# Optimization experiments

Hardware: AMD Instinct MI355X
Metric: run time of the kernel (lower is better)

Reference implementation:

```python
import jax, jax.numpy as jnp
import numpy as np

N = 100000   # nodes
E = 1600000  # edges (avg degree 16)
D = 128      # in = hid = out dim
EPS = 1e-5   # BatchNorm eps


def setup_inputs() -> dict:
    key = jax.random.key(0)
    ks = jax.random.split(key, 14)
    x = jax.random.normal(ks[0], (N, D), dtype=jnp.float32)
    row = jax.random.randint(ks[1], (E,), 0, N, dtype=jnp.int32)
    col = jax.random.randint(ks[2], (E,), 0, N, dtype=jnp.int32)
    edge_weight = jax.random.uniform(ks[3], (E,), dtype=jnp.float32)
    s = 1.0 / np.sqrt(D)
    W0 = jax.random.uniform(ks[4], (D, D), jnp.float32, -s, s)
    b0 = jax.random.uniform(ks[5], (D,), jnp.float32, -s, s)
    W1 = jax.random.uniform(ks[6], (D, D), jnp.float32, -s, s)
    b1 = jax.random.uniform(ks[7], (D,), jnp.float32, -s, s)
    W2 = jax.random.uniform(ks[8], (D, D), jnp.float32, -s, s)
    b2 = jax.random.uniform(ks[9], (D,), jnp.float32, -s, s)
    g0 = jnp.ones((D,), jnp.float32); be0 = jnp.zeros((D,), jnp.float32)
    g1 = jnp.ones((D,), jnp.float32); be1 = jnp.zeros((D,), jnp.float32)
    return {"x": x, "edge_weight": edge_weight,
            "W0": W0, "b0": b0, "g0": g0, "be0": be0,
            "W1": W1, "b1": b1, "g1": g1, "be1": be1,
            "W2": W2, "b2": b2, "row": row, "col": col}


def _spmm(edge_weight, row, col, h):
    # (A_norm @ h) with A in COO: out[r] = sum_e w_e * h[col_e] for row_e == r
    return jax.ops.segment_sum(edge_weight[:, None] * h[col], row, num_segments=N)


def _bn(h, gamma, beta):
    # BatchNorm1d, training-mode stats (biased variance), over the node axis
    m = h.mean(axis=0)
    v = h.var(axis=0)
    return gamma * (h - m) * jax.lax.rsqrt(v + EPS) + beta


def reference(x, edge_weight, W0, b0, g0, be0, W1, b1, g1, be1, W2, b2, row, col):
    # hidden block 1: SpMM(A, Linear(h)) -> BN -> ReLU (dropout p=0)
    h = jax.nn.relu(_bn(_spmm(edge_weight, row, col, x @ W0 + b0), g0, be0))
    # hidden block 2
    h = jax.nn.relu(_bn(_spmm(edge_weight, row, col, h @ W1 + b1), g1, be1))
    # final layer: SpMM(A, Linear(h)), no BN/activation
    return _spmm(edge_weight, row, col, h @ W2 + b2)
```

## Files before the change

kernel.cpp:

```cpp
#include <hip/hip_runtime.h>
#include <cstddef>

#define DD 128
#define EPS 1e-5f

typedef short short8 __attribute__((ext_vector_type(8)));
typedef float float4v __attribute__((ext_vector_type(4)));

__device__ __forceinline__ unsigned short f2bf(float f) {
    union { float f; unsigned int u; } x; x.f = f;
    unsigned int r = x.u + 0x7fffu + ((x.u >> 16) & 1u);
    return (unsigned short)(r >> 16);
}
__device__ __forceinline__ float bfhi2f(unsigned int hi_bits) {
    union { unsigned int u; float f; } x; x.u = hi_bits;
    return x.f;
}


__global__ void hist_kernel(const int* __restrict__ row, int* __restrict__ deg, int E) {
    int e = blockIdx.x * blockDim.x + threadIdx.x;
    if (e < E) atomicAdd(&deg[row[e]], 1);
}

__global__ void scanA_kernel(const int* __restrict__ deg, int* __restrict__ tmp,
                             int* __restrict__ bsum, int n) {
    __shared__ int s[1024];
    int tid = threadIdx.x;
    int gid = blockIdx.x * 1024 + tid;
    int v = (gid < n) ? deg[gid] : 0;
    s[tid] = v;
    __syncthreads();
    for (int off = 1; off < 1024; off <<= 1) {
        int t = s[tid];
        int u = (tid >= off) ? s[tid - off] : 0;
        __syncthreads();
        s[tid] = t + u;
        __syncthreads();
    }
    if (gid < n) tmp[gid] = s[tid];
    if (tid == 1023) bsum[blockIdx.x] = s[1023];
}

__global__ void scanB_kernel(const int* __restrict__ bsum, int* __restrict__ boff,
                             int* __restrict__ row_start, int nb, int n) {
    __shared__ int s[128];
    int tid = threadIdx.x;
    int v = (tid < nb) ? bsum[tid] : 0;
    s[tid] = v;
    __syncthreads();
    for (int off = 1; off < 128; off <<= 1) {
        int t = s[tid];
        int u = (tid >= off) ? s[tid - off] : 0;
        __syncthreads();
        s[tid] = t + u;
        __syncthreads();
    }
    if (tid < nb) boff[tid] = s[tid] - v;
    if (tid == nb - 1) row_start[n] = s[tid];
}

__global__ void scanC_kernel(const int* __restrict__ deg, const int* __restrict__ tmp,
                             const int* __restrict__ boff, int* __restrict__ row_start,
                             int* __restrict__ cursor, int n) {
    int gid = blockIdx.x * 1024 + threadIdx.x;
    if (gid < n) {
        int rs = tmp[gid] - deg[gid] + boff[blockIdx.x];
        row_start[gid] = rs;
        cursor[gid] = rs;
    }
}


__global__ void bcur_init_kernel(const int* __restrict__ row_start,
                                 int* __restrict__ bcur, int nb) {
    int b = blockIdx.x * 256 + threadIdx.x;
    if (b < nb) bcur[b] = row_start[b << 8];
}

__global__ __launch_bounds__(256) void scatter_phase1_kernel(
    const int* __restrict__ row, const int* __restrict__ col,
    const float* __restrict__ ew, int* __restrict__ bcur,
    unsigned long long* __restrict__ ebuf2, int E, int nbuck) {
    __shared__ int hist[512];
    __shared__ int cur[512];
    int tid = threadIdx.x;
    int b = blockIdx.x;
    int C = (E + gridDim.x - 1) / gridDim.x;
    int e0 = b * C, e1 = min(E, e0 + C);
    for (int t = tid; t < nbuck; t += 256) hist[t] = 0;
    __syncthreads();
    for (int e = e0 + tid; e < e1; e += 256)
        atomicAdd(&hist[row[e] >> 8], 1);
    __syncthreads();
    for (int i = tid; i < nbuck; i += 256) {
        int t = i + b * 37;
        t -= (t >= nbuck) ? nbuck * (t / nbuck) : 0;
        int h = hist[t];
        cur[t] = h ? atomicAdd(&bcur[t], h) : 0;
    }
    __syncthreads();
    for (int e = e0 + tid; e < e1; e += 256) {
        int r = row[e];
        int bk = r >> 8;
        int pos = atomicAdd(&cur[bk], 1);
        unsigned long long pk = (unsigned long long)((unsigned int)col[e]
                              | ((unsigned int)(r & 255) << 24))
                              | ((unsigned long long)__float_as_uint(ew[e]) << 32);
        ebuf2[pos] = pk;
    }
}

#define P2CAP 6144

__global__ __launch_bounds__(256) void scatter_phase2_kernel(
    const unsigned long long* __restrict__ ebuf2, const int* __restrict__ row_start,
    int* __restrict__ cursor, unsigned long long* __restrict__ ebuf, int N) {
    __shared__ int cur[256];
    __shared__ unsigned long long outb[P2CAP];
    int b = blockIdx.x;
    int r_lo = b << 8;
    int r_hi = min(N, r_lo + 256);
    int e_lo = row_start[r_lo];
    int e_hi = row_start[r_hi];
    int cnt = e_hi - e_lo;
    int tid = threadIdx.x;
    if (cnt <= P2CAP) {
        int r = r_lo + tid;
        cur[tid] = (r < N) ? (row_start[r] - e_lo) : 0;
        __syncthreads();
        for (int i = e_lo + tid; i < e_hi; i += 256) {
            unsigned long long pk = ebuf2[i];
            int rl = (int)((unsigned int)(pk >> 24) & 255u);
            int pos = atomicAdd(&cur[rl], 1);
            outb[pos] = pk & 0xFFFFFFFF0001FFFFull;
        }
        __syncthreads();
        for (int i = tid; i < cnt; i += 256)
            ebuf[e_lo + i] = outb[i];
    } else {
        for (int i = e_lo + tid; i < e_hi; i += 256) {
            unsigned long long pk = ebuf2[i];
            int rl = (int)((unsigned int)(pk >> 24) & 255u);
            int pos = atomicAdd(&cursor[r_lo + rl], 1);
            ebuf[pos] = pk & 0xFFFFFFFF0001FFFFull;
        }
    }
}


__global__ void convw_kernel(const float* __restrict__ W0, const float* __restrict__ W1,
                             const float* __restrict__ W2, unsigned short* __restrict__ T0,
                             unsigned short* __restrict__ T1, unsigned short* __restrict__ T2) {
    const float* W = (blockIdx.y == 0) ? W0 : (blockIdx.y == 1) ? W1 : W2;
    unsigned short* T = (blockIdx.y == 0) ? T0 : (blockIdx.y == 1) ? T1 : T2;
    int gid = blockIdx.x * 256 + threadIdx.x;
    int k = gid >> 7, n = gid & 127;
    T[n * DD + k] = f2bf(W[k * DD + n]);
}


__global__ __launch_bounds__(256) void gemm_mfma_f32_kernel(
    const float* __restrict__ A, const unsigned short* __restrict__ Wt,
    const float* __restrict__ bias, unsigned short* __restrict__ H, int nrows)
{
    __shared__ unsigned short Asl[64][136];
    __shared__ unsigned short Wsl[128][136];

    const int tid  = threadIdx.x;
    const int row0 = blockIdx.x * 64;

    for (int i = tid; i < 2048; i += 256) {
        int r = i >> 4, off = (i & 15) * 8;
        *(uint4*)&Wsl[r][off] = *(const uint4*)(Wt + (size_t)r * DD + off);
    }
    for (int i = tid; i < 2048; i += 256) {
        int r = i >> 5, off4 = i & 31;
        int grow = row0 + r;
        float4 v = make_float4(0.f, 0.f, 0.f, 0.f);
        if (grow < nrows)
            v = *(const float4*)(A + (size_t)grow * DD + off4 * 4);
        ushort4 p;
        p.x = f2bf(v.x); p.y = f2bf(v.y); p.z = f2bf(v.z); p.w = f2bf(v.w);
        *(ushort4*)&Asl[r][off4 * 4] = p;
    }
    __syncthreads();

    const int w = tid >> 6, lane = tid & 63;
    const int m = lane & 15, q = lane >> 4;

    short8 afr[4];
    #pragma unroll
    for (int c = 0; c < 4; ++c)
        afr[c] = *(const short8*)&Asl[w * 16 + m][c * 32 + q * 8];

    float4v acc[8];
    #pragma unroll
    for (int t = 0; t < 8; ++t) acc[t] = (float4v){0.f, 0.f, 0.f, 0.f};

    #pragma unroll
    for (int t = 0; t < 8; ++t) {
        #pragma unroll
        for (int c = 0; c < 4; ++c) {
            short8 bfr = *(const short8*)&Wsl[t * 16 + m][c * 32 + q * 8];
            acc[t] = __builtin_amdgcn_mfma_f32_16x16x32_bf16(afr[c], bfr, acc[t], 0, 0, 0);
        }
    }

    #pragma unroll
    for (int t = 0; t < 8; ++t) {
        float bv = bias[t * 16 + m];
        #pragma unroll
        for (int i = 0; i < 4; ++i)
            Asl[w * 16 + q * 4 + i][t * 16 + m] = f2bf(acc[t][i] + bv);
    }
    __syncthreads();

    for (int i = tid; i < 1024; i += 256) {
        int r = i >> 4, off = (i & 15) * 8;
        if (row0 + r < nrows)
            *(uint4*)(H + (size_t)(row0 + r) * DD + off) = *(const uint4*)&Asl[r][off];
    }
}


__global__ __launch_bounds__(256) void gemm_mfma_bf16_kernel(
    const unsigned int* __restrict__ A, const unsigned short* __restrict__ Wt,
    const float* __restrict__ bias,
    const float* __restrict__ sums, const float* __restrict__ g,
    const float* __restrict__ be,
    unsigned short* __restrict__ H, int nrows)
{
    __shared__ unsigned short Asl[64][136];
    __shared__ unsigned short Wsl[128][136];
    __shared__ float scl_s[128], sft_s[128];

    const int tid  = threadIdx.x;
    const int row0 = blockIdx.x * 64;

    if (tid < 128) {
        float inv_n = 1.0f / (float)nrows;
        float mean = sums[tid] * inv_n;
        float var = sums[128 + tid] * inv_n - mean * mean;
        float rstd = rsqrtf(var + EPS);
        float sc = g[tid] * rstd;
        scl_s[tid] = sc;
        sft_s[tid] = be[tid] - mean * sc;
    }

    for (int i = tid; i < 2048; i += 256) {
        int r = i >> 4, off = (i & 15) * 8;
        *(uint4*)&Wsl[r][off] = *(const uint4*)(Wt + (size_t)r * DD + off);
    }
    __syncthreads();

    for (int i = tid; i < 1024; i += 256) {
        int r = i >> 4, ch = (i & 15) * 8;
        int grow = row0 + r;
        uint4 u = make_uint4(0, 0, 0, 0);
        if (grow < nrows)
            u = *(const uint4*)(A + (size_t)grow * 64 + (ch >> 1));
        unsigned int uu[4] = {u.x, u.y, u.z, u.w};
        unsigned int outp[4];
        #pragma unroll
        for (int j = 0; j < 4; ++j) {
            float vx = bfhi2f(uu[j] << 16);
            float vy = bfhi2f(uu[j] & 0xffff0000u);
            int k = ch + j * 2;
            vx = fmaxf(0.f, vx * scl_s[k] + sft_s[k]);
            vy = fmaxf(0.f, vy * scl_s[k + 1] + sft_s[k + 1]);
            outp[j] = (unsigned int)f2bf(vx) | ((unsigned int)f2bf(vy) << 16);
        }
        *(uint4*)&Asl[r][ch] = *(const uint4*)outp;
    }
    __syncthreads();

    const int w = tid >> 6, lane = tid & 63;
    const int m = lane & 15, q = lane >> 4;

    short8 afr[4];
    #pragma unroll
    for (int c = 0; c < 4; ++c)
        afr[c] = *(const short8*)&Asl[w * 16 + m][c * 32 + q * 8];

    float4v acc[8];
    #pragma unroll
    for (int t = 0; t < 8; ++t) acc[t] = (float4v){0.f, 0.f, 0.f, 0.f};

    #pragma unroll
    for (int t = 0; t < 8; ++t) {
        #pragma unroll
        for (int c = 0; c < 4; ++c) {
            short8 bfr = *(const short8*)&Wsl[t * 16 + m][c * 32 + q * 8];
            acc[t] = __builtin_amdgcn_mfma_f32_16x16x32_bf16(afr[c], bfr, acc[t], 0, 0, 0);
        }
    }

    #pragma unroll
    for (int t = 0; t < 8; ++t) {
        float bv = bias[t * 16 + m];
        #pragma unroll
        for (int i = 0; i < 4; ++i)
            Asl[w * 16 + q * 4 + i][t * 16 + m] = f2bf(acc[t][i] + bv);
    }
    __syncthreads();

    for (int i = tid; i < 1024; i += 256) {
        int r = i >> 4, off = (i & 15) * 8;
        if (row0 + r < nrows)
            *(uint4*)(H + (size_t)(row0 + r) * DD + off) = *(const uint4*)&Asl[r][off];
    }
}


__global__ __launch_bounds__(256, 8) void spmm_bf16_kernel(
    const unsigned short* __restrict__ H, const int* __restrict__ row_start,
    const unsigned long long* __restrict__ ebuf,
    float* __restrict__ Sf, unsigned int* __restrict__ Sb, int writeBF, int N, int K)
{
    const int lane = threadIdx.x & 63;
    const int g = lane >> 4;
    const int p = lane & 15;
    const int wave = (blockIdx.x << 2) | (threadIdx.x >> 6);
    int r0 = wave * K;
    if (r0 >= N) return;
    int r1 = min(N, r0 + K);

    const unsigned short* Hp = H + p * 8;
    const unsigned long long* Ep = ebuf + g;

    for (int r = r0; r < r1; ++r) {
        int e = row_start[r];
        const int e1 = row_start[r + 1];
        float acc[8];
        #pragma unroll
        for (int j = 0; j < 8; ++j) acc[j] = 0.f;

        for (; e + 15 < e1; e += 16) {
            unsigned long long pk[4];
            #pragma unroll
            for (int j = 0; j < 4; ++j)
                pk[j] = __builtin_nontemporal_load(Ep + e + j * 4);
            uint4 u[4];
            #pragma unroll
            for (int j = 0; j < 4; ++j)
                u[j] = *(const uint4*)(Hp + (size_t)(unsigned int)pk[j] * DD);
            #pragma unroll
            for (int j = 0; j < 4; ++j) {
                float wj = __uint_as_float((unsigned int)(pk[j] >> 32));
                unsigned int uu[4] = {u[j].x, u[j].y, u[j].z, u[j].w};
                #pragma unroll
                for (int q = 0; q < 4; ++q) {
                    acc[2 * q]     += wj * bfhi2f(uu[q] << 16);
                    acc[2 * q + 1] += wj * bfhi2f(uu[q] & 0xffff0000u);
                }
            }
        }
        for (; e + 7 < e1; e += 8) {
            unsigned long long pk[2];
            #pragma unroll
            for (int j = 0; j < 2; ++j)
                pk[j] = __builtin_nontemporal_load(Ep + e + j * 4);
            uint4 u[2];
            #pragma unroll
            for (int j = 0; j < 2; ++j)
                u[j] = *(const uint4*)(Hp + (size_t)(unsigned int)pk[j] * DD);
            #pragma unroll
            for (int j = 0; j < 2; ++j) {
                float wj = __uint_as_float((unsigned int)(pk[j] >> 32));
                unsigned int uu[4] = {u[j].x, u[j].y, u[j].z, u[j].w};
                #pragma unroll
                for (int q = 0; q < 4; ++q) {
                    acc[2 * q]     += wj * bfhi2f(uu[q] << 16);
                    acc[2 * q + 1] += wj * bfhi2f(uu[q] & 0xffff0000u);
                }
            }
        }
        if (e + 3 < e1) {
            unsigned long long pk = __builtin_nontemporal_load(Ep + e);
            uint4 u = *(const uint4*)(Hp + (size_t)(unsigned int)pk * DD);
            float wj = __uint_as_float((unsigned int)(pk >> 32));
            unsigned int uu[4] = {u.x, u.y, u.z, u.w};
            #pragma unroll
            for (int q = 0; q < 4; ++q) {
                acc[2 * q]     += wj * bfhi2f(uu[q] << 16);
                acc[2 * q + 1] += wj * bfhi2f(uu[q] & 0xffff0000u);
            }
            e += 4;
        }
        if (e < e1) {
            int idx = e + g;
            unsigned long long pk = (idx < e1) ? __builtin_nontemporal_load(&ebuf[idx]) : 0ull;
            uint4 u = *(const uint4*)(Hp + (size_t)(unsigned int)pk * DD);
            float wj = __uint_as_float((unsigned int)(pk >> 32));
            unsigned int uu[4] = {u.x, u.y, u.z, u.w};
            #pragma unroll
            for (int q = 0; q < 4; ++q) {
                acc[2 * q]     += wj * bfhi2f(uu[q] << 16);
                acc[2 * q + 1] += wj * bfhi2f(uu[q] & 0xffff0000u);
            }
        }

        #pragma unroll
        for (int j = 0; j < 8; ++j) {
            acc[j] += __shfl_xor(acc[j], 16);
            acc[j] += __shfl_xor(acc[j], 32);
        }

        if (g == 0) {
            if (writeBF) {
                unsigned int o[4];
                #pragma unroll
                for (int j = 0; j < 4; ++j)
                    o[j] = (unsigned int)f2bf(acc[2 * j])
                         | ((unsigned int)f2bf(acc[2 * j + 1]) << 16);
                *(uint4*)(Sb + (size_t)r * 64 + p * 4) = *(const uint4*)o;
            } else {
                float4 lo = make_float4(acc[0], acc[1], acc[2], acc[3]);
                float4 hi = make_float4(acc[4], acc[5], acc[6], acc[7]);
                *(float4*)(Sf + (size_t)r * DD + p * 8) = lo;
                *(float4*)(Sf + (size_t)r * DD + p * 8 + 4) = hi;
            }
        }
    }
}


__global__ void bn_stats_bf16_kernel(const unsigned int* __restrict__ Sb,
                                     float* __restrict__ sums, int n) {
    __shared__ float lsx[256], lsx2[256], lsy[256], lsy2[256];
    int tid = threadIdx.x;
    int c2 = tid & 63;
    float sx = 0.f, sx2 = 0.f, sy = 0.f, sy2 = 0.f;
    int total = n * 64;
    for (int i = blockIdx.x * 256 + tid; i < total; i += 256 * 256) {
        unsigned int u = Sb[i];
        float vx = bfhi2f(u << 16);
        float vy = bfhi2f(u & 0xffff0000u);
        sx += vx; sx2 += vx * vx;
        sy += vy; sy2 += vy * vy;
    }
    lsx[tid] = sx; lsx2[tid] = sx2; lsy[tid] = sy; lsy2[tid] = sy2;
    __syncthreads();
    if (tid < 64) {
        sx  = lsx[tid]  + lsx[tid + 64]  + lsx[tid + 128]  + lsx[tid + 192];
        sx2 = lsx2[tid] + lsx2[tid + 64] + lsx2[tid + 128] + lsx2[tid + 192];
        sy  = lsy[tid]  + lsy[tid + 64]  + lsy[tid + 128]  + lsy[tid + 192];
        sy2 = lsy2[tid] + lsy2[tid + 64] + lsy2[tid + 128] + lsy2[tid + 192];
        atomicAdd(&sums[2 * c2], sx);
        atomicAdd(&sums[2 * c2 + 1], sy);
        atomicAdd(&sums[128 + 2 * c2], sx2);
        atomicAdd(&sums[129 + 2 * c2], sy2);
    }
}


extern "C" void kernel_launch(void* const* d_in, const int* in_sizes, int n_in,
                              void* d_out, int out_size, void* d_ws, size_t ws_size,
                              hipStream_t stream) {
    const float* x   = (const float*)d_in[0];
    const float* ew  = (const float*)d_in[1];
    const float* W0  = (const float*)d_in[2];
    const float* b0  = (const float*)d_in[3];
    const float* g0  = (const float*)d_in[4];
    const float* be0 = (const float*)d_in[5];
    const float* W1  = (const float*)d_in[6];
    const float* b1  = (const float*)d_in[7];
    const float* g1  = (const float*)d_in[8];
    const float* be1 = (const float*)d_in[9];
    const float* W2  = (const float*)d_in[10];
    const float* b2  = (const float*)d_in[11];
    const int* row   = (const int*)d_in[12];
    const int* col   = (const int*)d_in[13];

    const int N = in_sizes[0] / DD;
    const int E = in_sizes[1];
    float* out = (float*)d_out;

    char* w = (char*)d_ws;
    unsigned short* H   = (unsigned short*)w; w += (size_t)N * DD * 2;
    unsigned int* Sb    = (unsigned int*)w;   w += (size_t)N * 64 * 4;
    unsigned long long* ebuf = (unsigned long long*)w; w += (size_t)E * 8;
    unsigned short* Wt0 = (unsigned short*)w; w += DD * DD * 2;
    unsigned short* Wt1 = (unsigned short*)w; w += DD * DD * 2;
    unsigned short* Wt2 = (unsigned short*)w; w += DD * DD * 2;
    float* sums         = (float*)w;          w += 256 * 4;
    int*   deg          = (int*)w;            w += (size_t)N * 4;
    int*   tmp          = (int*)w;            w += (size_t)N * 4;
    int*   cursor       = (int*)w;            w += (size_t)N * 4;
    int*   bsum         = (int*)w;            w += 128 * 4;
    int*   boff         = (int*)w;            w += 128 * 4;
    int*   row_start    = (int*)w;            w += (size_t)(N + 1) * 4;

    unsigned long long* ebuf2 = (unsigned long long*)Sb;
    int* bcur = tmp;
    int nbuck = (N + 255) >> 8;

    hipMemsetAsync(deg, 0, (size_t)N * 4, stream);
    hist_kernel<<<(E + 255) / 256, 256, 0, stream>>>(row, deg, E);
    int NB = (N + 1023) / 1024;
    scanA_kernel<<<NB, 1024, 0, stream>>>(deg, tmp, bsum, N);
    scanB_kernel<<<1, 128, 0, stream>>>(bsum, boff, row_start, NB, N);
    scanC_kernel<<<NB, 1024, 0, stream>>>(deg, tmp, boff, row_start, cursor, N);
    bcur_init_kernel<<<(nbuck + 255) / 256, 256, 0, stream>>>(row_start, bcur, nbuck);
    scatter_phase1_kernel<<<256, 256, 0, stream>>>(row, col, ew, bcur, ebuf2, E, nbuck);
    scatter_phase2_kernel<<<nbuck, 256, 0, stream>>>(ebuf2, row_start, cursor, ebuf, N);

    convw_kernel<<<dim3(64, 3), 256, 0, stream>>>(W0, W1, W2, Wt0, Wt1, Wt2);

    int gblocks = (N + 63) / 64;

    const int SPMM_BLOCKS = 2048;
    const int totalWaves = SPMM_BLOCKS * 4;
    const int K = (N + totalWaves - 1) / totalWaves;

    gemm_mfma_f32_kernel<<<gblocks, 256, 0, stream>>>(x, Wt0, b0, H, N);
    spmm_bf16_kernel<<<SPMM_BLOCKS, 256, 0, stream>>>(H, row_start, ebuf, nullptr, Sb, 1, N, K);
    hipMemsetAsync(sums, 0, 256 * 4, stream);
    bn_stats_bf16_kernel<<<256, 256, 0, stream>>>(Sb, sums, N);

    gemm_mfma_bf16_kernel<<<gblocks, 256, 0, stream>>>(Sb, Wt1, b1, sums, g0, be0, H, N);
    spmm_bf16_kernel<<<SPMM_BLOCKS, 256, 0, stream>>>(H, row_start, ebuf, nullptr, Sb, 1, N, K);
    hipMemsetAsync(sums, 0, 256 * 4, stream);
    bn_stats_bf16_kernel<<<256, 256, 0, stream>>>(Sb, sums, N);

    gemm_mfma_bf16_kernel<<<gblocks, 256, 0, stream>>>(Sb, Wt2, b2, sums, g1, be1, H, N);
    spmm_bf16_kernel<<<SPMM_BLOCKS, 256, 0, stream>>>(H, row_start, ebuf, out, nullptr, 0, N, K);
}
```

Baseline: 576.8 us.

## Pad CSR rows to multiples of four and stream edges with software prefetch

Each row's edge count is rounded up to a multiple of four during the scan, and the padding slots are zero-filled in scatter phase 2. This makes every row a whole number of 4-edge groups. The SpMM kernel drops the per-row unrolled loops and tail handling. It becomes a single continuous loop over the wave's edge range that prefetches the next edge packets and H rows one to two steps ahead, flushing each row when its padded end is reached. The trade-offs are up to three dummy gathers of H row 0 per row, extra zeroing work, a larger edge buffer, and scatter_phase1 and phase2 now relying on the final bucket cursors for the real edge counts.

Result: no change. 583.6 us (+1.2%).

```diff
diff --git a/kernel.cpp b/kernel.cpp
--- a/kernel.cpp
+++ b/kernel.cpp
@@ -28,7 +28,7 @@
     __shared__ int s[1024];
     int tid = threadIdx.x;
     int gid = blockIdx.x * 1024 + tid;
-    int v = (gid < n) ? deg[gid] : 0;
+    int v = (gid < n) ? ((deg[gid] + 3) & ~3) : 0;
     s[tid] = v;
     __syncthreads();
     for (int off = 1; off < 1024; off <<= 1) {
@@ -65,7 +65,8 @@
                              int* __restrict__ cursor, int n) {
     int gid = blockIdx.x * 1024 + threadIdx.x;
     if (gid < n) {
-        int rs = tmp[gid] - deg[gid] + boff[blockIdx.x];
+        int pd = (deg[gid] + 3) & ~3;
+        int rs = tmp[gid] - pd + boff[blockIdx.x];
         row_start[gid] = rs;
         cursor[gid] = rs;
     }
@@ -115,7 +116,8 @@
 
 __global__ __launch_bounds__(256) void scatter_phase2_kernel(
     const unsigned long long* __restrict__ ebuf2, const int* __restrict__ row_start,
-    int* __restrict__ cursor, unsigned long long* __restrict__ ebuf, int N) {
+    const int* __restrict__ bcur_final, int* __restrict__ cursor,
+    unsigned long long* __restrict__ ebuf, int N) {
     __shared__ int cur[256];
     __shared__ unsigned long long outb[P2CAP];
     int b = blockIdx.x;
@@ -123,23 +125,28 @@
     int r_hi = min(N, r_lo + 256);
     int e_lo = row_start[r_lo];
     int e_hi = row_start[r_hi];
-    int cnt = e_hi - e_lo;
+    int cnt_pad = e_hi - e_lo;
+    int cnt_real = bcur_final[b] - e_lo;
     int tid = threadIdx.x;
-    if (cnt <= P2CAP) {
+    if (cnt_pad <= P2CAP) {
         int r = r_lo + tid;
         cur[tid] = (r < N) ? (row_start[r] - e_lo) : 0;
-        __syncthreads();
-        for (int i = e_lo + tid; i < e_hi; i += 256) {
+        for (int i = tid; i < cnt_pad; i += 256) outb[i] = 0ull;
+        __syncthreads();
+        for (int i = e_lo + tid; i < e_lo + cnt_real; i += 256) {
             unsigned long long pk = ebuf2[i];
             int rl = (int)((unsigned int)(pk >> 24) & 255u);
             int pos = atomicAdd(&cur[rl], 1);
             outb[pos] = pk & 0xFFFFFFFF0001FFFFull;
         }
         __syncthreads();
-        for (int i = tid; i < cnt; i += 256)
+        for (int i = tid; i < cnt_pad; i += 256)
             ebuf[e_lo + i] = outb[i];
     } else {
-        for (int i = e_lo + tid; i < e_hi; i += 256) {
+        for (int i = e_lo + tid; i < e_hi; i += 256) ebuf[i] = 0ull;
+        __threadfence();
+        __syncthreads();
+        for (int i = e_lo + tid; i < e_lo + cnt_real; i += 256) {
             unsigned long long pk = ebuf2[i];
             int rl = (int)((unsigned int)(pk >> 24) & 255u);
             int pos = atomicAdd(&cursor[r_lo + rl], 1);
@@ -314,9 +321,10 @@
 
 
 __global__ __launch_bounds__(256, 8) void spmm_bf16_kernel(
-    const unsigned short* __restrict__ H, const int* __restrict__ row_start,
+    const unsigned short* __restrict__ H, const int* __restrict__ ps,
     const unsigned long long* __restrict__ ebuf,
-    float* __restrict__ Sf, unsigned int* __restrict__ Sb, int writeBF, int N, int K)
+    float* __restrict__ Sf, unsigned int* __restrict__ Sb, int writeBF,
+    int N, int K)
 {
     const int lane = threadIdx.x & 63;
     const int g = lane >> 4;
@@ -327,101 +335,79 @@
     int r1 = min(N, r0 + K);
 
     const unsigned short* Hp = H + p * 8;
-    const unsigned long long* Ep = ebuf + g;
-
-    for (int r = r0; r < r1; ++r) {
-        int e = row_start[r];
-        const int e1 = row_start[r + 1];
-        float acc[8];
+
+    int r = r0;
+    int e = ps[r0];
+    const int eEnd = ps[r1];
+
+    while (r < r1 && ps[r + 1] == e) {
+        if (g == 0) {
+            if (writeBF) {
+                uint4 z = make_uint4(0, 0, 0, 0);
+                *(uint4*)(Sb + (size_t)r * 64 + p * 4) = z;
+            } else {
+                float4 z = make_float4(0.f, 0.f, 0.f, 0.f);
+                *(float4*)(Sf + (size_t)r * DD + p * 8) = z;
+                *(float4*)(Sf + (size_t)r * DD + p * 8 + 4) = z;
+            }
+        }
+        ++r;
+    }
+    if (r >= r1) return;
+    int next_end = ps[r + 1];
+
+    unsigned long long pk_cur = __builtin_nontemporal_load(&ebuf[e + g]);
+    int i1 = e + 4; i1 = (i1 < eEnd) ? i1 : e;
+    unsigned long long pk_nxt = __builtin_nontemporal_load(&ebuf[i1 + g]);
+    uint4 u_cur = *(const uint4*)(Hp + (size_t)(unsigned int)pk_cur * DD);
+
+    float acc[8];
+    #pragma unroll
+    for (int j = 0; j < 8; ++j) acc[j] = 0.f;
+
+    for (; e < eEnd; e += 4) {
+        int i2 = e + 8; i2 = (i2 < eEnd) ? i2 : e;
+        unsigned long long pk_f = __builtin_nontemporal_load(&ebuf[i2 + g]);
+        uint4 u_nxt = *(const uint4*)(Hp + (size_t)(unsigned int)pk_nxt * DD);
+        float wj = __uint_as_float((unsigned int)(pk_cur >> 32));
+        unsigned int uu[4] = {u_cur.x, u_cur.y, u_cur.z, u_cur.w};
         #pragma unroll
-        for (int j = 0; j < 8; ++j) acc[j] = 0.f;
-
-        for (; e + 15 < e1; e += 16) {
-            unsigned long long pk[4];
+        for (int q4 = 0; q4 < 4; ++q4) {
+            acc[2 * q4]     += wj * bfhi2f(uu[q4] << 16);
+            acc[2 * q4 + 1] += wj * bfhi2f(uu[q4] & 0xffff0000u);
+        }
+
+        while (e + 4 == next_end) {
             #pragma unroll
-            for (int j = 0; j < 4; ++j)
-                pk[j] = __builtin_nontemporal_load(Ep + e + j * 4);
-            uint4 u[4];
-            #pragma unroll
-            for (int j = 0; j < 4; ++j)
-                u[j] = *(const uint4*)(Hp + (size_t)(unsigned int)pk[j] * DD);
-            #pragma unroll
-            for (int j = 0; j < 4; ++j) {
-                float wj = __uint_as_float((unsigned int)(pk[j] >> 32));
-                unsigned int uu[4] = {u[j].x, u[j].y, u[j].z, u[j].w};
-                #pragma unroll
-                for (int q = 0; q < 4; ++q) {
-                    acc[2 * q]     += wj * bfhi2f(uu[q] << 16);
-                    acc[2 * q + 1] += wj * bfhi2f(uu[q] & 0xffff0000u);
+            for (int j = 0; j < 8; ++j) {
+                acc[j] += __shfl_xor(acc[j], 16);
+                acc[j] += __shfl_xor(acc[j], 32);
+            }
+            if (g == 0) {
+                if (writeBF) {
+                    unsigned int o[4];
+                    #pragma unroll
+                    for (int j = 0; j < 4; ++j)
+                        o[j] = (unsigned int)f2bf(acc[2 * j])
+                             | ((unsigned int)f2bf(acc[2 * j + 1]) << 16);
+                    *(uint4*)(Sb + (size_t)r * 64 + p * 4) = *(const uint4*)o;
+                } else {
+                    float4 lo = make_float4(acc[0], acc[1], acc[2], acc[3]);
+                    float4 hi = make_float4(acc[4], acc[5], acc[6], acc[7]);
+                    *(float4*)(Sf + (size_t)r * DD + p * 8) = lo;
+                    *(float4*)(Sf + (size_t)r * DD + p * 8 + 4) = hi;
                 }
             }
-        }
-        for (; e + 7 < e1; e += 8) {
-            unsigned long long pk[2];
             #pragma unroll
-            for (int j = 0; j < 2; ++j)
-                pk[j] = __builtin_nontemporal_load(Ep + e + j * 4);
-            uint4 u[2];
-            #pragma unroll
-            for (int j = 0; j < 2; ++j)
-                u[j] = *(const uint4*)(Hp + (size_t)(unsigned int)pk[j] * DD);
-            #pragma unroll
-            for (int j = 0; j < 2; ++j) {
-                float wj = __uint_as_float((unsigned int)(pk[j] >> 32));
-                unsigned int uu[4] = {u[j].x, u[j].y, u[j].z, u[j].w};
-                #pragma unroll
-                for (int q = 0; q < 4; ++q) {
-                    acc[2 * q]     += wj * bfhi2f(uu[q] << 16);
-                    acc[2 * q + 1] += wj * bfhi2f(uu[q] & 0xffff0000u);
-                }
-            }
-        }
-        if (e + 3 < e1) {
-            unsigned long long pk = __builtin_nontemporal_load(Ep + e);
-            uint4 u = *(const uint4*)(Hp + (size_t)(unsigned int)pk * DD);
-            float wj = __uint_as_float((unsigned int)(pk >> 32));
-            unsigned int uu[4] = {u.x, u.y, u.z, u.w};
-            #pragma unroll
-            for (int q = 0; q < 4; ++q) {
-                acc[2 * q]     += wj * bfhi2f(uu[q] << 16);
-                acc[2 * q + 1] += wj * bfhi2f(uu[q] & 0xffff0000u);
-            }
-            e += 4;
-        }
-        if (e < e1) {
-            int idx = e + g;
-            unsigned long long pk = (idx < e1) ? __builtin_nontemporal_load(&ebuf[idx]) : 0ull;
-            uint4 u = *(const uint4*)(Hp + (size_t)(unsigned int)pk * DD);
-            float wj = __uint_as_float((unsigned int)(pk >> 32));
-            unsigned int uu[4] = {u.x, u.y, u.z, u.w};
-            #pragma unroll
-            for (int q = 0; q < 4; ++q) {
-                acc[2 * q]     += wj * bfhi2f(uu[q] << 16);
-                acc[2 * q + 1] += wj * bfhi2f(uu[q] & 0xffff0000u);
-            }
-        }
-
-        #pragma unroll
-        for (int j = 0; j < 8; ++j) {
-            acc[j] += __shfl_xor(acc[j], 16);
-            acc[j] += __shfl_xor(acc[j], 32);
-        }
-
-        if (g == 0) {
-            if (writeBF) {
-                unsigned int o[4];
-                #pragma unroll
-                for (int j = 0; j < 4; ++j)
-                    o[j] = (unsigned int)f2bf(acc[2 * j])
-                         | ((unsigned int)f2bf(acc[2 * j + 1]) << 16);
-                *(uint4*)(Sb + (size_t)r * 64 + p * 4) = *(const uint4*)o;
-            } else {
-                float4 lo = make_float4(acc[0], acc[1], acc[2], acc[3]);
-                float4 hi = make_float4(acc[4], acc[5], acc[6], acc[7]);
-                *(float4*)(Sf + (size_t)r * DD + p * 8) = lo;
-                *(float4*)(Sf + (size_t)r * DD + p * 8 + 4) = hi;
-            }
-        }
+            for (int j = 0; j < 8; ++j) acc[j] = 0.f;
+            ++r;
+            if (r >= r1) break;
+            next_end = ps[r + 1];
+        }
+
+        pk_cur = pk_nxt;
+        u_cur  = u_nxt;
+        pk_nxt = pk_f;
     }
 }
 
@@ -477,10 +463,12 @@
     const int E = in_sizes[1];
     float* out = (float*)d_out;
 
+    const size_t EPADCAP = (size_t)E + 3 * (size_t)N + 64;
+
     char* w = (char*)d_ws;
     unsigned short* H   = (unsigned short*)w; w += (size_t)N * DD * 2;
     unsigned int* Sb    = (unsigned int*)w;   w += (size_t)N * 64 * 4;
-    unsigned long long* ebuf = (unsigned long long*)w; w += (size_t)E * 8;
+    unsigned long long* ebuf = (unsigned long long*)w; w += EPADCAP * 8;
     unsigned short* Wt0 = (unsigned short*)w; w += DD * DD * 2;
     unsigned short* Wt1 = (unsigned short*)w; w += DD * DD * 2;
     unsigned short* Wt2 = (unsigned short*)w; w += DD * DD * 2;
@@ -504,7 +492,7 @@
     scanC_kernel<<<NB, 1024, 0, stream>>>(deg, tmp, boff, row_start, cursor, N);
     bcur_init_kernel<<<(nbuck + 255) / 256, 256, 0, stream>>>(row_start, bcur, nbuck);
     scatter_phase1_kernel<<<256, 256, 0, stream>>>(row, col, ew, bcur, ebuf2, E, nbuck);
-    scatter_phase2_kernel<<<nbuck, 256, 0, stream>>>(ebuf2, row_start, cursor, ebuf, N);
+    scatter_phase2_kernel<<<nbuck, 256, 0, stream>>>(ebuf2, row_start, bcur, cursor, ebuf, N);
 
     convw_kernel<<<dim3(64, 3), 256, 0, stream>>>(W0, W1, W2, Wt0, Wt1, Wt2);
 
```
